# Kernel tuning notes

Hardware: AMD Instinct MI355X
Metric: run time of the kernel (lower is better)

## Reference

```python
import jax, jax.numpy as jnp
import numpy as np

B, Q, S = 4, 16384, 4
QD = FD = HD = 256
H = W = 128
OFFSET_SCALE = 0.05


def grid_sample_bilinear(feats, grid):
    # feats [B,C,H,W], grid [B,N,2] (x,y) normalized coords, align_corners=True, zeros padding
    Bb, C, Hh, Ww = feats.shape
    x = (grid[..., 0] + 1.0) * 0.5 * (Ww - 1)
    y = (grid[..., 1] + 1.0) * 0.5 * (Hh - 1)
    x0 = jnp.floor(x)
    y0 = jnp.floor(y)
    wx1 = x - x0
    wy1 = y - y0
    x0i = x0.astype(jnp.int32)
    y0i = y0.astype(jnp.int32)
    flat = feats.reshape(Bb, C, Hh * Ww)

    def corner(xi, yi, w):
        valid = ((xi >= 0) & (xi < Ww) & (yi >= 0) & (yi < Hh)).astype(feats.dtype)
        idx = jnp.clip(yi, 0, Hh - 1) * Ww + jnp.clip(xi, 0, Ww - 1)
        vals = jnp.take_along_axis(flat, idx[:, None, :], axis=2)  # [B,C,N]
        return vals * (w * valid)[:, None, :]

    return (corner(x0i, y0i, (1 - wx1) * (1 - wy1))
            + corner(x0i + 1, y0i, wx1 * (1 - wy1))
            + corner(x0i, y0i + 1, (1 - wx1) * wy1)
            + corner(x0i + 1, y0i + 1, wx1 * wy1))  # [B,C,N]


def setup_inputs() -> dict:
    key = jax.random.key(0)
    ks = jax.random.split(key, 12)
    queries = jax.random.normal(ks[0], (B, Q, QD), jnp.float32)
    ref_points = jax.random.uniform(ks[1], (B, Q, 2), jnp.float32, -0.95, 0.95)
    feature_map = jax.random.normal(ks[2], (B, FD, H, W), jnp.float32)
    valid_mask = jax.random.randint(ks[3], (B, Q), 0, 10) > 0
    s = 0.02
    Wq = jax.random.normal(ks[4], (QD, HD), jnp.float32) * s
    bq = jnp.zeros((HD,), jnp.float32)
    Wf = jax.random.normal(ks[5], (FD, HD), jnp.float32) * s  # 1x1 conv weight
    bf = jnp.zeros((HD,), jnp.float32)
    Wo = jax.random.normal(ks[6], (QD, 2 * S), jnp.float32) * s
    bo = jnp.zeros((2 * S,), jnp.float32)
    Ww = jax.random.normal(ks[7], (QD, S), jnp.float32) * s
    bw = jnp.zeros((S,), jnp.float32)
    W1 = jax.random.normal(ks[8], (2 * HD, HD), jnp.float32) * s
    b1 = jnp.zeros((HD,), jnp.float32)
    W2 = jax.random.normal(ks[9], (HD, HD), jnp.float32) * s
    b2 = jnp.zeros((HD,), jnp.float32)
    return dict(queries=queries, ref_points=ref_points, feature_map=feature_map,
                valid_mask=valid_mask, Wq=Wq, bq=bq, Wf=Wf, bf=bf, Wo=Wo, bo=bo,
                Ww=Ww, bw=bw, W1=W1, b1=b1, W2=W2, b2=b2)


def reference(queries, ref_points, feature_map, valid_mask,
              Wq, bq, Wf, bf, Wo, bo, Ww, bw, W1, b1, W2, b2):
    Bb, Qq, _ = queries.shape
    Ss = Ww.shape[1]
    Hd = Wq.shape[1]
    pq = queries @ Wq + bq                                    # [B,Q,HD]
    pf = jnp.einsum('bchw,cd->bdhw', feature_map, Wf) + bf[None, :, None, None]
    off = jnp.tanh(queries @ Wo + bo).reshape(Bb, Qq, Ss, 2) * OFFSET_SCALE
    w = jax.nn.softmax(queries @ Ww + bw, axis=-1)            # [B,Q,S]
    grid = jnp.clip(ref_points[:, :, None, :] + off, -1.2, 1.2).reshape(Bb, Qq * Ss, 2)
    sampled = grid_sample_bilinear(pf, grid)                  # [B,HD,Q*S]
    sampled = sampled.reshape(Bb, Hd, Qq, Ss).transpose(0, 2, 3, 1)  # [B,Q,S,HD]
    m = valid_mask.astype(sampled.dtype)
    sampled = sampled * m[:, :, None, None]
    w = w * m[:, :, None]
    w = w / jnp.clip(jnp.sum(w, axis=-1, keepdims=True), 1e-6, None)
    ctx = jnp.sum(sampled * w[..., None], axis=2)             # [B,Q,HD]
    ctx = ctx * m[:, :, None]
    pq = pq * m[:, :, None]
    hcat = jnp.concatenate([pq, ctx], axis=-1)                # [B,Q,2*HD]
    return jax.nn.relu(hcat @ W1 + b1) @ W2 + b2
```

## Files before the change

### kernel.cpp

```cpp
#include <hip/hip_runtime.h>
#include <hip/hip_bf16.h>
#include <math.h>


#define NQ 65536
#define OFFSET_SCALE 0.05f

typedef __bf16 bf16x8 __attribute__((ext_vector_type(8)));
typedef float f32x4 __attribute__((ext_vector_type(4)));
typedef float f32x2 __attribute__((ext_vector_type(2)));
typedef unsigned short u16x8 __attribute__((ext_vector_type(8)));

__device__ __forceinline__ float dot4(float4 a, float4 b) {
  return a.x * b.x + a.y * b.y + a.z * b.z + a.w * b.w;
}

__device__ __forceinline__ ushort f2bf(float f) {
  union { float f; unsigned u; } v; v.f = f;
  unsigned r = v.u + 0x7FFFu + ((v.u >> 16) & 1u);
  return (ushort)(r >> 16);
}

__device__ __forceinline__ f32x2 up2(unsigned u) {
  union { unsigned u; float f; } lo, hi;
  lo.u = u << 16;
  hi.u = u & 0xFFFF0000u;
  f32x2 r = {lo.f, hi.f};
  return r;
}

__device__ __forceinline__ unsigned pkbf(f32x2 v) {
  float2 f; f.x = v[0]; f.y = v[1];
  union { __hip_bfloat162 h; unsigned u; } x;
  x.h = __float22bfloat162_rn(f);
  return x.u;
}

__device__ __forceinline__ void gload16(const void* g, void* s) {
  __builtin_amdgcn_global_load_lds(
      (const __attribute__((address_space(1))) void*)g,
      (__attribute__((address_space(3))) void*)s, 16, 0, 0);
}

__global__ void __launch_bounds__(256) k_misc(
    const float* __restrict__ fm, ushort* __restrict__ fmT,
    const float* __restrict__ Wq, const float* __restrict__ Wf,
    const float* __restrict__ W1, const float* __restrict__ W2,
    const float* __restrict__ bq, const float* __restrict__ bf,
    ushort* __restrict__ ABt, ushort* __restrict__ W2t,
    float* __restrict__ uvec, float* __restrict__ vvec,
    const float* __restrict__ queries, const int* __restrict__ valid,
    const float* __restrict__ Wo, const float* __restrict__ bo,
    const float* __restrict__ Ww, const float* __restrict__ bw,
    float* __restrict__ proj, ushort* __restrict__ qraw) {
  __shared__ ushort tile[128][70];
  const int bid = blockIdx.x;
  const int t = threadIdx.x;

  if (bid < 49) {
    const int n = t;
    if (bid < 32) {
      const int k0 = bid * 16;
      const float* src = (bid < 16) ? (Wq + (size_t)k0 * 256)
                                    : (Wf + (size_t)(k0 - 256) * 256);
      const int joff = (bid < 16) ? 0 : 256;
      float acc[16];
#pragma unroll
      for (int r = 0; r < 16; ++r) acc[r] = 0.f;
#pragma unroll 4
      for (int j = 0; j < 256; ++j) {
        const float w = W1[(size_t)(j + joff) * 256 + n];
#pragma unroll
        for (int r = 0; r < 16; ++r) acc[r] = fmaf(src[r * 256 + j], w, acc[r]);
      }
      u16x8 o0, o1;
#pragma unroll
      for (int r = 0; r < 8; ++r) { o0[r] = f2bf(acc[r]); o1[r] = f2bf(acc[8 + r]); }
      *(u16x8*)(ABt + (size_t)n * 512 + k0) = o0;
      *(u16x8*)(ABt + (size_t)n * 512 + k0 + 8) = o1;
    } else if (bid == 32) {
      float su = 0.f, sv = 0.f;
      for (int j = 0; j < 256; ++j) {
        su = fmaf(bq[j], W1[(size_t)j * 256 + n], su);
        sv = fmaf(bf[j], W1[(size_t)(256 + j) * 256 + n], sv);
      }
      uvec[n] = su;
      vvec[n] = sv;
    } else {
      const int k0 = (bid - 33) * 16;
      u16x8 o0, o1;
#pragma unroll
      for (int r = 0; r < 8; ++r) {
        o0[r] = f2bf(W2[(size_t)(k0 + r) * 256 + n]);
        o1[r] = f2bf(W2[(size_t)(k0 + 8 + r) * 256 + n]);
      }
      *(u16x8*)(W2t + (size_t)n * 256 + k0) = o0;
      *(u16x8*)(W2t + (size_t)n * 256 + k0 + 8) = o1;
    }
    return;
  }

  const int r3 = bid - 49;
  if ((r3 % 3) == 0) {
    const int tb = r3 / 3;
    const int c0 = (tb & 3) * 64;
    const int y  = (tb >> 2) & 127;
    const int b  = tb >> 9;
#pragma unroll
    for (int rep = 0; rep < 32; ++rep) {
      const int idx = t + rep * 256;
      const int ci = idx >> 7, x = idx & 127;
      tile[x][ci] = f2bf(fm[(((size_t)(b * 256 + c0 + ci) * 128 + y) << 7) + x]);
    }
    __syncthreads();
#pragma unroll
    for (int rep = 0; rep < 4; ++rep) {
      const int idx = t + rep * 256;
      const int x = idx >> 3, c8 = idx & 7;
      const ushort4 a = *(const ushort4*)&tile[x][c8 * 8];
      const ushort4 b4 = *(const ushort4*)&tile[x][c8 * 8 + 4];
      const u16x8 o = {a.x, a.y, a.z, a.w, b4.x, b4.y, b4.z, b4.w};
      *(u16x8*)(fmT + (((size_t)((b * 128 + y) * 128 + x)) << 8) + c0 + c8 * 8) = o;
    }
  } else {
    const int blk = (r3 / 3) * 2 + (r3 % 3) - 1;
    float (*sW)[260] = (float(*)[260])&tile[0][0];
    float* sb = (float*)&tile[0][0] + 12 * 260;
    for (int i = t; i < 2048; i += 256) sW[i & 7][i >> 3] = Wo[i];
    for (int i = t; i < 1024; i += 256) sW[8 + (i & 3)][i >> 2] = Ww[i];
    if (t < 8) sb[t] = bo[t];
    else if (t < 12) sb[t] = bw[t - 8];
    __syncthreads();

    const int lane = t & 63, wv = t >> 6;
    const int ql = lane >> 4, kc = lane & 15;
    const int qi = blk * 16 + wv * 4 + ql;
    const float mf = (valid[qi] != 0) ? 1.0f : 0.0f;

    float4 qv[4];
#pragma unroll
    for (int i = 0; i < 4; ++i)
      qv[i] = *(const float4*)(queries + (size_t)qi * 256 + kc * 4 + i * 64);

    float pr[12];
#pragma unroll
    for (int j = 0; j < 12; ++j) {
      float s = 0.f;
#pragma unroll
      for (int i = 0; i < 4; ++i)
        s += dot4(qv[i], *(const float4*)&sW[j][kc * 4 + i * 64]);
      pr[j] = s;
    }
#pragma unroll
    for (int m = 1; m < 16; m <<= 1) {
#pragma unroll
      for (int j = 0; j < 12; ++j) pr[j] += __shfl_xor(pr[j], m, 64);
    }
    if (kc == 0) {
      float4* pp = (float4*)(proj + (size_t)qi * 16);
      const float4 o0 = {pr[0] + sb[0], pr[1] + sb[1], pr[2] + sb[2],  pr[3] + sb[3]};
      const float4 o1 = {pr[4] + sb[4], pr[5] + sb[5], pr[6] + sb[6],  pr[7] + sb[7]};
      const float4 o2 = {pr[8] + sb[8], pr[9] + sb[9], pr[10] + sb[10], pr[11] + sb[11]};
      pp[0] = o0; pp[1] = o1; pp[2] = o2;
    }
#pragma unroll
    for (int i = 0; i < 4; ++i) {
      ushort4 h;
      h.x = f2bf(qv[i].x * mf); h.y = f2bf(qv[i].y * mf);
      h.z = f2bf(qv[i].z * mf); h.w = f2bf(qv[i].w * mf);
      *(ushort4*)(qraw + (size_t)qi * 512 + kc * 4 + i * 64) = h;
    }
  }
}

__global__ void __launch_bounds__(256) k_gather(
    const float* __restrict__ proj, const float* __restrict__ ref,
    const int* __restrict__ valid, const ushort* __restrict__ fmT,
    ushort* __restrict__ qraw, float* __restrict__ cov) {
  const int t = threadIdx.x, lane = t & 63, wv = t >> 6;
  const int qs = lane >> 4;
  const int kc = lane & 15;
  const int xcd = blockIdx.x & 7;
  const int b = xcd >> 1;
  const int p = ((blockIdx.x >> 3) << 1) | (xcd & 1);
  const ushort* fmTb = fmT + ((size_t)b << 22);

#pragma unroll 1
  for (int it = 0; it < 2; ++it) {
    const int qi = b * 16384 + it * 8192 + p * 16 + wv * 4 + qs;
    const float mf = (valid[qi] != 0) ? 1.0f : 0.0f;
    const float4 pA = *(const float4*)(proj + (size_t)qi * 16);
    const float4 pB = *(const float4*)(proj + (size_t)qi * 16 + 4);
    const float4 pC = *(const float4*)(proj + (size_t)qi * 16 + 8);
    const float rx = ref[qi * 2], ry = ref[qi * 2 + 1];

    const float po[8] = {pA.x, pA.y, pA.z, pA.w, pB.x, pB.y, pB.z, pB.w};
    float o[8];
#pragma unroll
    for (int j = 0; j < 8; ++j) {
      const float x = po[j];
      const float e = __expf(2.0f * fabsf(x));
      const float th = 1.0f - 2.0f * __builtin_amdgcn_rcpf(e + 1.0f);
      o[j] = copysignf(th, x) * OFFSET_SCALE;
    }
    float wl[4] = {pC.x, pC.y, pC.z, pC.w};
    const float wmax = fmaxf(fmaxf(wl[0], wl[1]), fmaxf(wl[2], wl[3]));
    float wsum = 0.f;
#pragma unroll
    for (int j = 0; j < 4; ++j) { wl[j] = __expf(wl[j] - wmax); wsum += wl[j]; }
    const float winv = mf * __builtin_amdgcn_rcpf(wsum);

    f32x2 acc[8] = {};
    float cv = 0.f;

#define CORN(PIXPTR, CF)                                                     \
    do {                                                                     \
      const float cfv = (CF);                                                \
      const uint4 u0 = *(const uint4*)((PIXPTR) + kc * 8);                   \
      const uint4 u1 = *(const uint4*)((PIXPTR) + kc * 8 + 128);             \
      const f32x2 c2 = {cfv, cfv};                                           \
      acc[0] += c2 * up2(u0.x); acc[1] += c2 * up2(u0.y);                    \
      acc[2] += c2 * up2(u0.z); acc[3] += c2 * up2(u0.w);                    \
      acc[4] += c2 * up2(u1.x); acc[5] += c2 * up2(u1.y);                    \
      acc[6] += c2 * up2(u1.z); acc[7] += c2 * up2(u1.w);                    \
    } while (0)

#pragma unroll
    for (int s = 0; s < 4; ++s) {
      const float wgt = wl[s] * winv;
      const float gx = fminf(fmaxf(rx + o[2 * s],     -1.2f), 1.2f);
      const float gy = fminf(fmaxf(ry + o[2 * s + 1], -1.2f), 1.2f);
      const float xf = (gx + 1.0f) * 63.5f;
      const float yf = (gy + 1.0f) * 63.5f;
      const float x0f = floorf(xf), y0f = floorf(yf);
      const float wx = xf - x0f, wy = yf - y0f;
      const int x0 = (int)x0f, y0 = (int)y0f;
      const float wx0 = ((unsigned)x0 < 128u) ? (1.0f - wx) : 0.0f;
      const float wx1 = ((unsigned)(x0 + 1) < 128u) ? wx : 0.0f;
      const float wy0 = ((unsigned)y0 < 128u) ? (wgt * (1.0f - wy)) : 0.0f;
      const float wy1 = ((unsigned)(y0 + 1) < 128u) ? (wgt * wy) : 0.0f;
      const int xc0 = min(max(x0, 0), 127), xc1 = min(max(x0 + 1, 0), 127);
      const int yc0 = min(max(y0, 0), 127), yc1 = min(max(y0 + 1, 0), 127);
      cv += (wx0 + wx1) * (wy0 + wy1);
      const ushort* r0 = fmTb + ((size_t)yc0 << 15);
      const ushort* r1 = fmTb + ((size_t)yc1 << 15);
      CORN(r0 + (xc0 << 8), wy0 * wx0);
      CORN(r0 + (xc1 << 8), wy0 * wx1);
      CORN(r1 + (xc0 << 8), wy1 * wx0);
      CORN(r1 + (xc1 << 8), wy1 * wx1);
    }
#undef CORN

    uint4 w0, w1;
    w0.x = pkbf(acc[0]); w0.y = pkbf(acc[1]); w0.z = pkbf(acc[2]); w0.w = pkbf(acc[3]);
    w1.x = pkbf(acc[4]); w1.y = pkbf(acc[5]); w1.z = pkbf(acc[6]); w1.w = pkbf(acc[7]);
    *(uint4*)(qraw + (size_t)qi * 512 + 256 + kc * 8) = w0;
    *(uint4*)(qraw + (size_t)qi * 512 + 256 + 128 + kc * 8) = w1;
    if (kc == 0) cov[qi] = cv;
  }
}

__global__ void __launch_bounds__(256, 3) k_gemm_fused(
    const ushort* __restrict__ qraw, const ushort* __restrict__ ABt,
    const ushort* __restrict__ W2t, const int* __restrict__ valid,
    const float* __restrict__ cov, const float* __restrict__ uvec,
    const float* __restrict__ vvec, const float* __restrict__ b1,
    const float* __restrict__ b2, float* __restrict__ out) {
  __shared__ ushort As[64 * 32];
  __shared__ ushort Bs[256 * 32];
  __shared__ ushort Hs[64 * 256];
  const int t = threadIdx.x;
  const int m0 = blockIdx.x * 64;
  const int wn = t >> 6, lane = t & 63;
  const int lr = lane & 15, lg = lane >> 4;

  const int srow = t >> 2;
  const int schunk = ((t & 3) ^ ((srow >> 1) & 3)) * 8;
  const int swz = (lg ^ ((lr >> 1) & 3)) * 8;

  const ushort* ag = qraw + (size_t)(m0 + srow) * 512 + schunk;
  const ushort* bg = ABt + (size_t)srow * 512 + schunk;
  ushort* la = As + t * 8;
  ushort* lb = Bs + t * 8;

  f32x4 acc[4][4] = {};

  for (int k0 = 0; k0 < 512; k0 += 32) {
    __syncthreads();
    gload16(ag + k0, la);
    gload16(bg + k0, lb);
    gload16(bg + 64 * 512 + k0, lb + 2048);
    gload16(bg + 128 * 512 + k0, lb + 4096);
    gload16(bg + 192 * 512 + k0, lb + 6144);
    __syncthreads();
    bf16x8 af[4], bfr[4];
#pragma unroll
    for (int m = 0; m < 4; ++m)
      af[m] = *(const bf16x8*)(As + (m * 16 + lr) * 32 + swz);
#pragma unroll
    for (int n = 0; n < 4; ++n)
      bfr[n] = *(const bf16x8*)(Bs + (wn * 64 + n * 16 + lr) * 32 + swz);
#pragma unroll
    for (int m = 0; m < 4; ++m)
#pragma unroll
      for (int n = 0; n < 4; ++n)
        acc[m][n] = __builtin_amdgcn_mfma_f32_16x16x32_bf16(af[m], bfr[n], acc[m][n], 0, 0, 0);
  }

  {
    float uu[4], vv[4], bb[4];
#pragma unroll
    for (int n = 0; n < 4; ++n) {
      const int col = wn * 64 + n * 16 + lr;
      uu[n] = uvec[col]; vv[n] = vvec[col]; bb[n] = b1[col];
    }
#pragma unroll
    for (int m = 0; m < 4; ++m)
#pragma unroll
      for (int j = 0; j < 4; ++j) {
        const int row = m * 16 + lg * 4 + j;
        const float mfv = valid[m0 + row] ? 1.0f : 0.0f;
        const float cvr = cov[m0 + row];
#pragma unroll
        for (int n = 0; n < 4; ++n) {
          const int col = wn * 64 + n * 16 + lr;
          float r = acc[m][n][j] + mfv * uu[n] + cvr * vv[n] + bb[n];
          r = fmaxf(r, 0.0f);
          const int slot = (col >> 3) ^ (row & 7);
          Hs[row * 256 + slot * 8 + (col & 7)] = f2bf(r);
        }
      }
  }

  const ushort* cg = W2t + (size_t)srow * 256 + schunk;
#pragma unroll
  for (int m = 0; m < 4; ++m)
#pragma unroll
    for (int n = 0; n < 4; ++n) {
      f32x4 z = {0.f, 0.f, 0.f, 0.f};
      acc[m][n] = z;
    }

  for (int k0 = 0; k0 < 256; k0 += 32) {
    __syncthreads();
    gload16(cg + k0, lb);
    gload16(cg + 64 * 256 + k0, lb + 2048);
    gload16(cg + 128 * 256 + k0, lb + 4096);
    gload16(cg + 192 * 256 + k0, lb + 6144);
    __syncthreads();
    bf16x8 af[4], bfr[4];
#pragma unroll
    for (int m = 0; m < 4; ++m) {
      const int slot = ((k0 >> 3) + lg) ^ (lr & 7);
      af[m] = *(const bf16x8*)(Hs + (m * 16 + lr) * 256 + slot * 8);
    }
#pragma unroll
    for (int n = 0; n < 4; ++n)
      bfr[n] = *(const bf16x8*)(Bs + (wn * 64 + n * 16 + lr) * 32 + swz);
#pragma unroll
    for (int m = 0; m < 4; ++m)
#pragma unroll
      for (int n = 0; n < 4; ++n)
        acc[m][n] = __builtin_amdgcn_mfma_f32_16x16x32_bf16(af[m], bfr[n], acc[m][n], 0, 0, 0);
  }

  {
    float bb[4];
#pragma unroll
    for (int n = 0; n < 4; ++n) bb[n] = b2[wn * 64 + n * 16 + lr];
#pragma unroll
    for (int m = 0; m < 4; ++m)
#pragma unroll
      for (int j = 0; j < 4; ++j) {
        const int row = m0 + m * 16 + lg * 4 + j;
#pragma unroll
        for (int n = 0; n < 4; ++n)
          out[(size_t)row * 256 + wn * 64 + n * 16 + lr] = acc[m][n][j] + bb[n];
      }
  }
}

extern "C" void kernel_launch(void* const* d_in, const int* in_sizes, int n_in,
                              void* d_out, int out_size, void* d_ws, size_t ws_size,
                              hipStream_t stream) {
  const float* queries = (const float*)d_in[0];
  const float* ref     = (const float*)d_in[1];
  const float* fm      = (const float*)d_in[2];
  const int*   valid   = (const int*)d_in[3];
  const float* Wq = (const float*)d_in[4];
  const float* bq = (const float*)d_in[5];
  const float* Wf = (const float*)d_in[6];
  const float* bf = (const float*)d_in[7];
  const float* Wo = (const float*)d_in[8];
  const float* bo = (const float*)d_in[9];
  const float* Ww = (const float*)d_in[10];
  const float* bw = (const float*)d_in[11];
  const float* W1 = (const float*)d_in[12];
  const float* b1 = (const float*)d_in[13];
  const float* W2 = (const float*)d_in[14];
  const float* b2 = (const float*)d_in[15];
  float* out = (float*)d_out;

  char* ws = (char*)d_ws;
  ushort* qraw = (ushort*)ws;
  float*  cov  = (float*)(ws + 67108864);
  ushort* ABt  = (ushort*)(ws + 67108864 + 262144);
  ushort* W2t  = (ushort*)(ws + 67108864 + 524288);
  float*  uvec = (float*)(ws + 67108864 + 655360);
  float*  vvec = uvec + 256;

  ushort* fmT  = (ushort*)d_out;
  float*  proj = out + 9437184;

  k_misc<<<6193, 256, 0, stream>>>(fm, fmT, Wq, Wf, W1, W2, bq, bf, ABt, W2t,
                                   uvec, vvec, queries, valid, Wo, bo, Ww, bw,
                                   proj, qraw);
  k_gather<<<2048, 256, 0, stream>>>(proj, ref, valid, fmT, qraw, cov);
  k_gemm_fused<<<1024, 256, 0, stream>>>(qraw, ABt, W2t, valid, cov, uvec, vvec,
                                         b1, b2, out);
}
```

Measured before the change: 136.2 us.

## Use MFMA for query projections and vectorize swizzled feature-map transpose

The query offset/weight projection now runs as a bf16 MFMA over 64 queries per block instead of per-lane fp32 dot products followed by shuffle reductions. The feature-map transpose now uses float4 loads, bf16 packing and an XOR-swizzled LDS layout. The block split is rebalanced so k_misc launches about half as many blocks. Projections are now computed from bf16-rounded queries that have already been multiplied by the valid mask. This lowers precision, and invalid queries get bias-only projections, which the later masking should make harmless.

```diff
diff --git a/kernel.cpp b/kernel.cpp
--- a/kernel.cpp
+++ b/kernel.cpp
@@ -10,10 +10,6 @@
 typedef float f32x4 __attribute__((ext_vector_type(4)));
 typedef float f32x2 __attribute__((ext_vector_type(2)));
 typedef unsigned short u16x8 __attribute__((ext_vector_type(8)));
-
-__device__ __forceinline__ float dot4(float4 a, float4 b) {
-  return a.x * b.x + a.y * b.y + a.z * b.z + a.w * b.w;
-}
 
 __device__ __forceinline__ ushort f2bf(float f) {
   union { float f; unsigned u; } v; v.f = f;
@@ -29,8 +25,8 @@
   return r;
 }
 
-__device__ __forceinline__ unsigned pkbf(f32x2 v) {
-  float2 f; f.x = v[0]; f.y = v[1];
+__device__ __forceinline__ unsigned pkbf(float a, float b) {
+  float2 f; f.x = a; f.y = b;
   union { __hip_bfloat162 h; unsigned u; } x;
   x.h = __float22bfloat162_rn(f);
   return x.u;
@@ -53,7 +49,7 @@
     const float* __restrict__ Wo, const float* __restrict__ bo,
     const float* __restrict__ Ww, const float* __restrict__ bw,
     float* __restrict__ proj, ushort* __restrict__ qraw) {
-  __shared__ ushort tile[128][70];
+  __shared__ ushort smem[8192];
   const int bid = blockIdx.x;
   const int t = threadIdx.x;
 
@@ -101,74 +97,85 @@
   }
 
   const int r3 = bid - 49;
-  if ((r3 % 3) == 0) {
-    const int tb = r3 / 3;
+  if ((r3 % 3) < 2) {
+    const int tb = (r3 / 3) * 2 + (r3 % 3);
     const int c0 = (tb & 3) * 64;
     const int y  = (tb >> 2) & 127;
     const int b  = tb >> 9;
-#pragma unroll
-    for (int rep = 0; rep < 32; ++rep) {
-      const int idx = t + rep * 256;
-      const int ci = idx >> 7, x = idx & 127;
-      tile[x][ci] = f2bf(fm[(((size_t)(b * 256 + c0 + ci) * 128 + y) << 7) + x]);
+    const int xgi = t & 31, x4 = xgi * 4;
+    char* sm = (char*)smem;
+#pragma unroll
+    for (int p = 0; p < 2; ++p) {
+      const int cgi = (t >> 5) + p * 8;
+      const float* src = fm + ((size_t)(b * 256 + c0 + cgi * 4) * 128 + y) * 128 + x4;
+      const f32x4 q0 = *(const f32x4*)(src);
+      const f32x4 q1 = *(const f32x4*)(src + 16384);
+      const f32x4 q2 = *(const f32x4*)(src + 32768);
+      const f32x4 q3 = *(const f32x4*)(src + 49152);
+#pragma unroll
+      for (int i = 0; i < 4; ++i) {
+        const int x = x4 + i;
+        uint2 w;
+        w.x = pkbf(q0[i], q1[i]);
+        w.y = pkbf(q2[i], q3[i]);
+        const int slot = (cgi >> 1) ^ ((x >> 2) & 7);
+        *(uint2*)(sm + x * 128 + slot * 16 + (cgi & 1) * 8) = w;
+      }
     }
     __syncthreads();
 #pragma unroll
     for (int rep = 0; rep < 4; ++rep) {
       const int idx = t + rep * 256;
       const int x = idx >> 3, c8 = idx & 7;
-      const ushort4 a = *(const ushort4*)&tile[x][c8 * 8];
-      const ushort4 b4 = *(const ushort4*)&tile[x][c8 * 8 + 4];
-      const u16x8 o = {a.x, a.y, a.z, a.w, b4.x, b4.y, b4.z, b4.w};
-      *(u16x8*)(fmT + (((size_t)((b * 128 + y) * 128 + x)) << 8) + c0 + c8 * 8) = o;
+      const int slot = c8 ^ ((x >> 2) & 7);
+      const u16x8 v = *(const u16x8*)(sm + x * 128 + slot * 16);
+      *(u16x8*)(fmT + (((size_t)((b * 128 + y) * 128 + x)) << 8) + c0 + c8 * 8) = v;
     }
   } else {
-    const int blk = (r3 / 3) * 2 + (r3 % 3) - 1;
-    float (*sW)[260] = (float(*)[260])&tile[0][0];
-    float* sb = (float*)&tile[0][0] + 12 * 260;
-    for (int i = t; i < 2048; i += 256) sW[i & 7][i >> 3] = Wo[i];
-    for (int i = t; i < 1024; i += 256) sW[8 + (i & 3)][i >> 2] = Ww[i];
-    if (t < 8) sb[t] = bo[t];
-    else if (t < 12) sb[t] = bw[t - 8];
-    __syncthreads();
-
-    const int lane = t & 63, wv = t >> 6;
-    const int ql = lane >> 4, kc = lane & 15;
-    const int qi = blk * 16 + wv * 4 + ql;
+    const int qblk = r3 / 3;
+    ushort (*Bt)[264] = (ushort(*)[264])smem;
+    float* sbias = (float*)(smem + 4224);
+    {
+      const int col = t & 15, k0s = (t >> 4) * 16;
+#pragma unroll 4
+      for (int kk = 0; kk < 16; ++kk) {
+        const int k = k0s + kk;
+        float v = 0.f;
+        if (col < 8) v = Wo[k * 8 + col];
+        else if (col < 12) v = Ww[k * 4 + (col - 8)];
+        Bt[col][k] = f2bf(v);
+      }
+      if (t < 16) sbias[t] = (t < 8) ? bo[t] : ((t < 12) ? bw[t - 8] : 0.f);
+    }
+    __syncthreads();
+
+    const int lane = t & 63, w = t >> 6;
+    const int row = lane & 15;
+    const int g = lane >> 4;
+    const int qi = qblk * 64 + w * 16 + row;
     const float mf = (valid[qi] != 0) ? 1.0f : 0.0f;
-
-    float4 qv[4];
-#pragma unroll
-    for (int i = 0; i < 4; ++i)
-      qv[i] = *(const float4*)(queries + (size_t)qi * 256 + kc * 4 + i * 64);
-
-    float pr[12];
-#pragma unroll
-    for (int j = 0; j < 12; ++j) {
-      float s = 0.f;
-#pragma unroll
-      for (int i = 0; i < 4; ++i)
-        s += dot4(qv[i], *(const float4*)&sW[j][kc * 4 + i * 64]);
-      pr[j] = s;
-    }
-#pragma unroll
-    for (int m = 1; m < 16; m <<= 1) {
-#pragma unroll
-      for (int j = 0; j < 12; ++j) pr[j] += __shfl_xor(pr[j], m, 64);
-    }
-    if (kc == 0) {
-      float4* pp = (float4*)(proj + (size_t)qi * 16);
-      const float4 o0 = {pr[0] + sb[0], pr[1] + sb[1], pr[2] + sb[2],  pr[3] + sb[3]};
-      const float4 o1 = {pr[4] + sb[4], pr[5] + sb[5], pr[6] + sb[6],  pr[7] + sb[7]};
-      const float4 o2 = {pr[8] + sb[8], pr[9] + sb[9], pr[10] + sb[10], pr[11] + sb[11]};
-      pp[0] = o0; pp[1] = o1; pp[2] = o2;
-    }
-#pragma unroll
-    for (int i = 0; i < 4; ++i) {
-      ushort4 h;
-      h.x = f2bf(qv[i].x * mf); h.y = f2bf(qv[i].y * mf);
-      h.z = f2bf(qv[i].z * mf); h.w = f2bf(qv[i].w * mf);
-      *(ushort4*)(qraw + (size_t)qi * 512 + kc * 4 + i * 64) = h;
+    const float* qsrc = queries + (size_t)qi * 256 + g * 8;
+    ushort* qdst = qraw + (size_t)qi * 512 + g * 8;
+    f32x4 acc = {0.f, 0.f, 0.f, 0.f};
+#pragma unroll
+    for (int ks = 0; ks < 8; ++ks) {
+      const f32x4 a0 = *(const f32x4*)(qsrc + ks * 32);
+      const f32x4 a1 = *(const f32x4*)(qsrc + ks * 32 + 4);
+      uint4 qa;
+      qa.x = pkbf(a0[0] * mf, a0[1] * mf);
+      qa.y = pkbf(a0[2] * mf, a0[3] * mf);
+      qa.z = pkbf(a1[0] * mf, a1[1] * mf);
+      qa.w = pkbf(a1[2] * mf, a1[3] * mf);
+      *(uint4*)(qdst + ks * 32) = qa;
+      union { uint4 u; bf16x8 h; } cvt; cvt.u = qa;
+      const bf16x8 bfrag = *(const bf16x8*)&Bt[row][g * 8 + ks * 32];
+      acc = __builtin_amdgcn_mfma_f32_16x16x32_bf16(cvt.h, bfrag, acc, 0, 0, 0);
+    }
+    if (row < 12) {
+      const float bias = sbias[row];
+#pragma unroll
+      for (int j = 0; j < 4; ++j)
+        proj[(size_t)(qblk * 64 + w * 16 + g * 4 + j) * 16 + row] = acc[j] + bias;
     }
   }
 }
@@ -252,8 +259,10 @@
 #undef CORN
 
     uint4 w0, w1;
-    w0.x = pkbf(acc[0]); w0.y = pkbf(acc[1]); w0.z = pkbf(acc[2]); w0.w = pkbf(acc[3]);
-    w1.x = pkbf(acc[4]); w1.y = pkbf(acc[5]); w1.z = pkbf(acc[6]); w1.w = pkbf(acc[7]);
+    w0.x = pkbf(acc[0][0], acc[0][1]); w0.y = pkbf(acc[1][0], acc[1][1]);
+    w0.z = pkbf(acc[2][0], acc[2][1]); w0.w = pkbf(acc[3][0], acc[3][1]);
+    w1.x = pkbf(acc[4][0], acc[4][1]); w1.y = pkbf(acc[5][0], acc[5][1]);
+    w1.z = pkbf(acc[6][0], acc[6][1]); w1.w = pkbf(acc[7][0], acc[7][1]);
     *(uint4*)(qraw + (size_t)qi * 512 + 256 + kc * 8) = w0;
     *(uint4*)(qraw + (size_t)qi * 512 + 256 + 128 + kc * 8) = w1;
     if (kc == 0) cov[qi] = cv;
@@ -412,7 +421,7 @@
   ushort* fmT  = (ushort*)d_out;
   float*  proj = out + 9437184;
 
-  k_misc<<<6193, 256, 0, stream>>>(fm, fmT, Wq, Wf, W1, W2, bq, bf, ABt, W2t,
+  k_misc<<<3121, 256, 0, stream>>>(fm, fmT, Wq, Wf, W1, W2, bq, bf, ABt, W2t,
                                    uvec, vvec, queries, valid, Wo, bo, Ww, bw,
                                    proj, qraw);
   k_gather<<<2048, 256, 0, stream>>>(proj, ref, valid, fmT, qraw, cov);
```

Measured after the change: 145.6 us. 1.07x slower.

## Fuse bilinear gather into the two-layer GEMM kernel via shared-memory staging

Applied to the files above, without the earlier changes.

Merges the gather kernel into the fused GEMM kernel. Each block now samples the feature map for its own 64 query rows, packs the weighted context to bf16 and keeps it in shared memory, instead of writing it to a global qraw buffer and reading it back. Coverage values also stay in shared memory, and the first GEMM splits its K loop into a global half for the queries and an LDS half for the sampled context. This removes one launch and a large global round trip. In exchange the gather work is serialized before the MFMA loop inside each block, and workspace buffers are reshuffled, with proj now stored in the output buffer.

```diff
diff --git a/kernel.cpp b/kernel.cpp
--- a/kernel.cpp
+++ b/kernel.cpp
@@ -29,8 +29,8 @@
   return r;
 }
 
-__device__ __forceinline__ unsigned pkbf(f32x2 v) {
-  float2 f; f.x = v[0]; f.y = v[1];
+__device__ __forceinline__ unsigned pkbf(float a, float b) {
+  float2 f; f.x = a; f.y = b;
   union { __hip_bfloat162 h; unsigned u; } x;
   x.h = __float22bfloat162_rn(f);
   return x.u;
@@ -52,7 +52,7 @@
     const float* __restrict__ queries, const int* __restrict__ valid,
     const float* __restrict__ Wo, const float* __restrict__ bo,
     const float* __restrict__ Ww, const float* __restrict__ bw,
-    float* __restrict__ proj, ushort* __restrict__ qraw) {
+    float* __restrict__ projo, ushort* __restrict__ qhalf) {
   __shared__ ushort tile[128][70];
   const int bid = blockIdx.x;
   const int t = threadIdx.x;
@@ -157,7 +157,7 @@
       for (int j = 0; j < 12; ++j) pr[j] += __shfl_xor(pr[j], m, 64);
     }
     if (kc == 0) {
-      float4* pp = (float4*)(proj + (size_t)qi * 16);
+      float4* pp = (float4*)(projo + (size_t)qi * 256);
       const float4 o0 = {pr[0] + sb[0], pr[1] + sb[1], pr[2] + sb[2],  pr[3] + sb[3]};
       const float4 o1 = {pr[4] + sb[4], pr[5] + sb[5], pr[6] + sb[6],  pr[7] + sb[7]};
       const float4 o2 = {pr[8] + sb[8], pr[9] + sb[9], pr[10] + sb[10], pr[11] + sb[11]};
@@ -168,30 +168,42 @@
       ushort4 h;
       h.x = f2bf(qv[i].x * mf); h.y = f2bf(qv[i].y * mf);
       h.z = f2bf(qv[i].z * mf); h.w = f2bf(qv[i].w * mf);
-      *(ushort4*)(qraw + (size_t)qi * 512 + kc * 4 + i * 64) = h;
-    }
-  }
-}
-
-__global__ void __launch_bounds__(256) k_gather(
-    const float* __restrict__ proj, const float* __restrict__ ref,
-    const int* __restrict__ valid, const ushort* __restrict__ fmT,
-    ushort* __restrict__ qraw, float* __restrict__ cov) {
-  const int t = threadIdx.x, lane = t & 63, wv = t >> 6;
-  const int qs = lane >> 4;
-  const int kc = lane & 15;
-  const int xcd = blockIdx.x & 7;
-  const int b = xcd >> 1;
-  const int p = ((blockIdx.x >> 3) << 1) | (xcd & 1);
-  const ushort* fmTb = fmT + ((size_t)b << 22);
+      *(ushort4*)(qhalf + (size_t)qi * 256 + kc * 4 + i * 64) = h;
+    }
+  }
+}
+
+__global__ void __launch_bounds__(256, 3) k_fused(
+    const ushort* __restrict__ qhalf, const float* __restrict__ projo,
+    const float* __restrict__ ref, const int* __restrict__ valid,
+    const ushort* __restrict__ fmT, const ushort* __restrict__ ABt,
+    const ushort* __restrict__ W2t, const float* __restrict__ uvec,
+    const float* __restrict__ vvec, const float* __restrict__ b1,
+    const float* __restrict__ b2, float* __restrict__ out) {
+  __shared__ ushort As[64 * 32];
+  __shared__ ushort Bs[256 * 32];
+  __shared__ ushort RHs[64 * 256];
+  __shared__ float covs[64];
+
+  const int t = threadIdx.x;
+  const int bid = blockIdx.x;
+  const int xcd = bid & 7;
+  const int bb = xcd >> 1;
+  const int m0 = (bb * 256 + (((bid >> 3) << 1) | (xcd & 1))) * 64;
+  const ushort* fmTb = fmT + ((size_t)bb << 22);
+
+  const int wn = t >> 6, lane = t & 63;
+  const int lr = lane & 15, lg = lane >> 4;
+  const int qs = lane >> 4, kc = lane & 15;
 
 #pragma unroll 1
-  for (int it = 0; it < 2; ++it) {
-    const int qi = b * 16384 + it * 8192 + p * 16 + wv * 4 + qs;
+  for (int it = 0; it < 4; ++it) {
+    const int row = wn * 16 + it * 4 + qs;
+    const int qi = m0 + row;
     const float mf = (valid[qi] != 0) ? 1.0f : 0.0f;
-    const float4 pA = *(const float4*)(proj + (size_t)qi * 16);
-    const float4 pB = *(const float4*)(proj + (size_t)qi * 16 + 4);
-    const float4 pC = *(const float4*)(proj + (size_t)qi * 16 + 8);
+    const float4 pA = *(const float4*)(projo + (size_t)qi * 256);
+    const float4 pB = *(const float4*)(projo + (size_t)qi * 256 + 4);
+    const float4 pC = *(const float4*)(projo + (size_t)qi * 256 + 8);
     const float rx = ref[qi * 2], ry = ref[qi * 2 + 1];
 
     const float po[8] = {pA.x, pA.y, pA.z, pA.w, pB.x, pB.y, pB.z, pB.w};
@@ -252,40 +264,27 @@
 #undef CORN
 
     uint4 w0, w1;
-    w0.x = pkbf(acc[0]); w0.y = pkbf(acc[1]); w0.z = pkbf(acc[2]); w0.w = pkbf(acc[3]);
-    w1.x = pkbf(acc[4]); w1.y = pkbf(acc[5]); w1.z = pkbf(acc[6]); w1.w = pkbf(acc[7]);
-    *(uint4*)(qraw + (size_t)qi * 512 + 256 + kc * 8) = w0;
-    *(uint4*)(qraw + (size_t)qi * 512 + 256 + 128 + kc * 8) = w1;
-    if (kc == 0) cov[qi] = cv;
-  }
-}
-
-__global__ void __launch_bounds__(256, 3) k_gemm_fused(
-    const ushort* __restrict__ qraw, const ushort* __restrict__ ABt,
-    const ushort* __restrict__ W2t, const int* __restrict__ valid,
-    const float* __restrict__ cov, const float* __restrict__ uvec,
-    const float* __restrict__ vvec, const float* __restrict__ b1,
-    const float* __restrict__ b2, float* __restrict__ out) {
-  __shared__ ushort As[64 * 32];
-  __shared__ ushort Bs[256 * 32];
-  __shared__ ushort Hs[64 * 256];
-  const int t = threadIdx.x;
-  const int m0 = blockIdx.x * 64;
-  const int wn = t >> 6, lane = t & 63;
-  const int lr = lane & 15, lg = lane >> 4;
+    w0.x = pkbf(acc[0][0], acc[0][1]); w0.y = pkbf(acc[1][0], acc[1][1]);
+    w0.z = pkbf(acc[2][0], acc[2][1]); w0.w = pkbf(acc[3][0], acc[3][1]);
+    w1.x = pkbf(acc[4][0], acc[4][1]); w1.y = pkbf(acc[5][0], acc[5][1]);
+    w1.z = pkbf(acc[6][0], acc[6][1]); w1.w = pkbf(acc[7][0], acc[7][1]);
+    const int s0 = kc ^ (row & 7), s1 = (16 + kc) ^ (row & 7);
+    *(uint4*)(RHs + row * 256 + s0 * 8) = w0;
+    *(uint4*)(RHs + row * 256 + s1 * 8) = w1;
+    if (kc == 0) covs[row] = cv;
+  }
 
   const int srow = t >> 2;
   const int schunk = ((t & 3) ^ ((srow >> 1) & 3)) * 8;
   const int swz = (lg ^ ((lr >> 1) & 3)) * 8;
-
-  const ushort* ag = qraw + (size_t)(m0 + srow) * 512 + schunk;
+  const ushort* ag = qhalf + (size_t)(m0 + srow) * 256 + schunk;
   const ushort* bg = ABt + (size_t)srow * 512 + schunk;
   ushort* la = As + t * 8;
   ushort* lb = Bs + t * 8;
 
   f32x4 acc[4][4] = {};
 
-  for (int k0 = 0; k0 < 512; k0 += 32) {
+  for (int k0 = 0; k0 < 256; k0 += 32) {
     __syncthreads();
     gload16(ag + k0, la);
     gload16(bg + k0, lb);
@@ -307,6 +306,31 @@
         acc[m][n] = __builtin_amdgcn_mfma_f32_16x16x32_bf16(af[m], bfr[n], acc[m][n], 0, 0, 0);
   }
 
+  for (int k0 = 256; k0 < 512; k0 += 32) {
+    __syncthreads();
+    gload16(bg + k0, lb);
+    gload16(bg + 64 * 512 + k0, lb + 2048);
+    gload16(bg + 128 * 512 + k0, lb + 4096);
+    gload16(bg + 192 * 512 + k0, lb + 6144);
+    __syncthreads();
+    bf16x8 af[4], bfr[4];
+#pragma unroll
+    for (int m = 0; m < 4; ++m) {
+      const int slot = (((k0 - 256) >> 3) + lg) ^ (lr & 7);
+      af[m] = *(const bf16x8*)(RHs + (m * 16 + lr) * 256 + slot * 8);
+    }
+#pragma unroll
+    for (int n = 0; n < 4; ++n)
+      bfr[n] = *(const bf16x8*)(Bs + (wn * 64 + n * 16 + lr) * 32 + swz);
+#pragma unroll
+    for (int m = 0; m < 4; ++m)
+#pragma unroll
+      for (int n = 0; n < 4; ++n)
+        acc[m][n] = __builtin_amdgcn_mfma_f32_16x16x32_bf16(af[m], bfr[n], acc[m][n], 0, 0, 0);
+  }
+
+  __syncthreads();
+
   {
     float uu[4], vv[4], bb[4];
 #pragma unroll
@@ -320,14 +344,14 @@
       for (int j = 0; j < 4; ++j) {
         const int row = m * 16 + lg * 4 + j;
         const float mfv = valid[m0 + row] ? 1.0f : 0.0f;
-        const float cvr = cov[m0 + row];
+        const float cvr = covs[row];
 #pragma unroll
         for (int n = 0; n < 4; ++n) {
           const int col = wn * 64 + n * 16 + lr;
           float r = acc[m][n][j] + mfv * uu[n] + cvr * vv[n] + bb[n];
           r = fmaxf(r, 0.0f);
           const int slot = (col >> 3) ^ (row & 7);
-          Hs[row * 256 + slot * 8 + (col & 7)] = f2bf(r);
+          RHs[row * 256 + slot * 8 + (col & 7)] = f2bf(r);
         }
       }
   }
@@ -352,7 +376,7 @@
 #pragma unroll
     for (int m = 0; m < 4; ++m) {
       const int slot = ((k0 >> 3) + lg) ^ (lr & 7);
-      af[m] = *(const bf16x8*)(Hs + (m * 16 + lr) * 256 + slot * 8);
+      af[m] = *(const bf16x8*)(RHs + (m * 16 + lr) * 256 + slot * 8);
     }
 #pragma unroll
     for (int n = 0; n < 4; ++n)
@@ -402,20 +426,18 @@
   float* out = (float*)d_out;
 
   char* ws = (char*)d_ws;
-  ushort* qraw = (ushort*)ws;
-  float*  cov  = (float*)(ws + 67108864);
-  ushort* ABt  = (ushort*)(ws + 67108864 + 262144);
-  ushort* W2t  = (ushort*)(ws + 67108864 + 524288);
-  float*  uvec = (float*)(ws + 67108864 + 655360);
-  float*  vvec = uvec + 256;
-
-  ushort* fmT  = (ushort*)d_out;
-  float*  proj = out + 9437184;
+  ushort* qhalf = (ushort*)ws;
+  ushort* fmT   = (ushort*)(ws + 33554432);
+  ushort* ABt   = (ushort*)(ws + 67108864);
+  ushort* W2t   = (ushort*)(ws + 67371008);
+  float*  uvec  = (float*)(ws + 67502080);
+  float*  vvec  = uvec + 256;
+
+  float* projo = out;
 
   k_misc<<<6193, 256, 0, stream>>>(fm, fmT, Wq, Wf, W1, W2, bq, bf, ABt, W2t,
                                    uvec, vvec, queries, valid, Wo, bo, Ww, bw,
-                                   proj, qraw);
-  k_gather<<<2048, 256, 0, stream>>>(proj, ref, valid, fmT, qraw, cov);
-  k_gemm_fused<<<1024, 256, 0, stream>>>(qraw, ABt, W2t, valid, cov, uvec, vvec,
-                                         b1, b2, out);
-}
+                                   projo, qhalf);
+  k_fused<<<1024, 256, 0, stream>>>(qhalf, projo, ref, valid, fmT, ABt, W2t,
+                                    uvec, vvec, b1, b2, out);
+}
```

After: 138.3 us. Within noise of the previous version (+1.5%).

## Split query and gathered halves into separate buffers, reuse output as scratch

Applied to the files above, without the earlier changes.

The combined bf16 A-operand buffer is split in two. The masked-query half goes to a compact workspace buffer, and the gathered-context half plus the small projection vector are written into the output buffer as scratch, laid out so each row's context data sits in the region that GEMM block later overwrites. The GEMM picks its K-slice source from one buffer or the other, and `__restrict__` is dropped from the aliased pointers. This reorganises the intermediate memory layout, likely to improve cache and TLB locality. The risk is that a GEMM block overwrites output rows that another block is still reading as context, which is safe only if each block reads and writes exactly its own rows.

```diff
diff --git a/kernel.cpp b/kernel.cpp
--- a/kernel.cpp
+++ b/kernel.cpp
@@ -29,8 +29,8 @@
   return r;
 }
 
-__device__ __forceinline__ unsigned pkbf(f32x2 v) {
-  float2 f; f.x = v[0]; f.y = v[1];
+__device__ __forceinline__ unsigned pkbf(float a, float b) {
+  float2 f; f.x = a; f.y = b;
   union { __hip_bfloat162 h; unsigned u; } x;
   x.h = __float22bfloat162_rn(f);
   return x.u;
@@ -52,7 +52,7 @@
     const float* __restrict__ queries, const int* __restrict__ valid,
     const float* __restrict__ Wo, const float* __restrict__ bo,
     const float* __restrict__ Ww, const float* __restrict__ bw,
-    float* __restrict__ proj, ushort* __restrict__ qraw) {
+    float* __restrict__ projo, ushort* __restrict__ qhalf) {
   __shared__ ushort tile[128][70];
   const int bid = blockIdx.x;
   const int t = threadIdx.x;
@@ -157,7 +157,7 @@
       for (int j = 0; j < 12; ++j) pr[j] += __shfl_xor(pr[j], m, 64);
     }
     if (kc == 0) {
-      float4* pp = (float4*)(proj + (size_t)qi * 16);
+      float4* pp = (float4*)(projo + (size_t)qi * 256 + 128);
       const float4 o0 = {pr[0] + sb[0], pr[1] + sb[1], pr[2] + sb[2],  pr[3] + sb[3]};
       const float4 o1 = {pr[4] + sb[4], pr[5] + sb[5], pr[6] + sb[6],  pr[7] + sb[7]};
       const float4 o2 = {pr[8] + sb[8], pr[9] + sb[9], pr[10] + sb[10], pr[11] + sb[11]};
@@ -168,15 +168,15 @@
       ushort4 h;
       h.x = f2bf(qv[i].x * mf); h.y = f2bf(qv[i].y * mf);
       h.z = f2bf(qv[i].z * mf); h.w = f2bf(qv[i].w * mf);
-      *(ushort4*)(qraw + (size_t)qi * 512 + kc * 4 + i * 64) = h;
+      *(ushort4*)(qhalf + (size_t)qi * 256 + kc * 4 + i * 64) = h;
     }
   }
 }
 
 __global__ void __launch_bounds__(256) k_gather(
-    const float* __restrict__ proj, const float* __restrict__ ref,
+    const float* __restrict__ projo, const float* __restrict__ ref,
     const int* __restrict__ valid, const ushort* __restrict__ fmT,
-    ushort* __restrict__ qraw, float* __restrict__ cov) {
+    ushort* __restrict__ rawd, float* __restrict__ cov) {
   const int t = threadIdx.x, lane = t & 63, wv = t >> 6;
   const int qs = lane >> 4;
   const int kc = lane & 15;
@@ -189,9 +189,9 @@
   for (int it = 0; it < 2; ++it) {
     const int qi = b * 16384 + it * 8192 + p * 16 + wv * 4 + qs;
     const float mf = (valid[qi] != 0) ? 1.0f : 0.0f;
-    const float4 pA = *(const float4*)(proj + (size_t)qi * 16);
-    const float4 pB = *(const float4*)(proj + (size_t)qi * 16 + 4);
-    const float4 pC = *(const float4*)(proj + (size_t)qi * 16 + 8);
+    const float4 pA = *(const float4*)(projo + (size_t)qi * 256 + 128);
+    const float4 pB = *(const float4*)(projo + (size_t)qi * 256 + 132);
+    const float4 pC = *(const float4*)(projo + (size_t)qi * 256 + 136);
     const float rx = ref[qi * 2], ry = ref[qi * 2 + 1];
 
     const float po[8] = {pA.x, pA.y, pA.z, pA.w, pB.x, pB.y, pB.z, pB.w};
@@ -252,20 +252,23 @@
 #undef CORN
 
     uint4 w0, w1;
-    w0.x = pkbf(acc[0]); w0.y = pkbf(acc[1]); w0.z = pkbf(acc[2]); w0.w = pkbf(acc[3]);
-    w1.x = pkbf(acc[4]); w1.y = pkbf(acc[5]); w1.z = pkbf(acc[6]); w1.w = pkbf(acc[7]);
-    *(uint4*)(qraw + (size_t)qi * 512 + 256 + kc * 8) = w0;
-    *(uint4*)(qraw + (size_t)qi * 512 + 256 + 128 + kc * 8) = w1;
+    w0.x = pkbf(acc[0][0], acc[0][1]); w0.y = pkbf(acc[1][0], acc[1][1]);
+    w0.z = pkbf(acc[2][0], acc[2][1]); w0.w = pkbf(acc[3][0], acc[3][1]);
+    w1.x = pkbf(acc[4][0], acc[4][1]); w1.y = pkbf(acc[5][0], acc[5][1]);
+    w1.z = pkbf(acc[6][0], acc[6][1]); w1.w = pkbf(acc[7][0], acc[7][1]);
+    *(uint4*)(rawd + (size_t)qi * 512 + kc * 8) = w0;
+    *(uint4*)(rawd + (size_t)qi * 512 + 128 + kc * 8) = w1;
     if (kc == 0) cov[qi] = cv;
   }
 }
 
 __global__ void __launch_bounds__(256, 3) k_gemm_fused(
-    const ushort* __restrict__ qraw, const ushort* __restrict__ ABt,
-    const ushort* __restrict__ W2t, const int* __restrict__ valid,
-    const float* __restrict__ cov, const float* __restrict__ uvec,
-    const float* __restrict__ vvec, const float* __restrict__ b1,
-    const float* __restrict__ b2, float* __restrict__ out) {
+    const ushort* __restrict__ qhalf, const ushort* rawd,
+    const ushort* __restrict__ ABt, const ushort* __restrict__ W2t,
+    const int* __restrict__ valid, const float* __restrict__ cov,
+    const float* __restrict__ uvec, const float* __restrict__ vvec,
+    const float* __restrict__ b1, const float* __restrict__ b2,
+    float* out) {
   __shared__ ushort As[64 * 32];
   __shared__ ushort Bs[256 * 32];
   __shared__ ushort Hs[64 * 256];
@@ -278,7 +281,8 @@
   const int schunk = ((t & 3) ^ ((srow >> 1) & 3)) * 8;
   const int swz = (lg ^ ((lr >> 1) & 3)) * 8;
 
-  const ushort* ag = qraw + (size_t)(m0 + srow) * 512 + schunk;
+  const ushort* agq = qhalf + (size_t)(m0 + srow) * 256 + schunk;
+  const ushort* agr = rawd  + (size_t)(m0 + srow) * 512 + schunk;
   const ushort* bg = ABt + (size_t)srow * 512 + schunk;
   ushort* la = As + t * 8;
   ushort* lb = Bs + t * 8;
@@ -287,7 +291,7 @@
 
   for (int k0 = 0; k0 < 512; k0 += 32) {
     __syncthreads();
-    gload16(ag + k0, la);
+    gload16((k0 < 256) ? (agq + k0) : (agr + (k0 - 256)), la);
     gload16(bg + k0, lb);
     gload16(bg + 64 * 512 + k0, lb + 2048);
     gload16(bg + 128 * 512 + k0, lb + 4096);
@@ -402,20 +406,21 @@
   float* out = (float*)d_out;
 
   char* ws = (char*)d_ws;
-  ushort* qraw = (ushort*)ws;
-  float*  cov  = (float*)(ws + 67108864);
-  ushort* ABt  = (ushort*)(ws + 67108864 + 262144);
-  ushort* W2t  = (ushort*)(ws + 67108864 + 524288);
-  float*  uvec = (float*)(ws + 67108864 + 655360);
-  float*  vvec = uvec + 256;
-
-  ushort* fmT  = (ushort*)d_out;
-  float*  proj = out + 9437184;
+  ushort* qhalf = (ushort*)ws;
+  ushort* fmT   = (ushort*)(ws + 33554432);
+  ushort* ABt   = (ushort*)(ws + 67108864);
+  ushort* W2t   = (ushort*)(ws + 67371008);
+  float*  uvec  = (float*)(ws + 67502080);
+  float*  vvec  = uvec + 256;
+  float*  cov   = (float*)(ws + 67504128);
+
+  float*  projo = out;
+  ushort* rawd  = (ushort*)d_out;
 
   k_misc<<<6193, 256, 0, stream>>>(fm, fmT, Wq, Wf, W1, W2, bq, bf, ABt, W2t,
                                    uvec, vvec, queries, valid, Wo, bo, Ww, bw,
-                                   proj, qraw);
-  k_gather<<<2048, 256, 0, stream>>>(proj, ref, valid, fmT, qraw, cov);
-  k_gemm_fused<<<1024, 256, 0, stream>>>(qraw, ABt, W2t, valid, cov, uvec, vvec,
-                                         b1, b2, out);
-}
+                                   projo, qhalf);
+  k_gather<<<2048, 256, 0, stream>>>(projo, ref, valid, fmT, rawd, cov);
+  k_gemm_fused<<<1024, 256, 0, stream>>>(qhalf, rawd, ABt, W2t, valid, cov,
+                                         uvec, vvec, b1, b2, out);
+}
```

Result: no change. 138.7 us (+1.8%).
